# Performance work log

Hardware: AMD Instinct MI355X
Metric: run time of the kernel (lower is better)

Reference implementation:

```python
import jax, jax.numpy as jnp
import numpy as np

B, L, D, V, O = 512, 256, 256, 100000, 1000  # L must equal D (see MaxPool1d(kernel_size=D) + squeeze)


def setup_inputs() -> dict:
    key = jax.random.key(0)
    k1, k2, k3, k4, k5 = jax.random.split(key, 5)
    input_sentence = jax.random.randint(k1, (B, L), 0, V)
    emb_weight = jax.random.normal(k2, (V, D), dtype=jnp.float32) * 0.02
    # xavier_uniform for W_b: bound = sqrt(6/(D+D))
    bound = float(np.sqrt(6.0 / (D + D)))
    W_b = jax.random.uniform(k3, (D, D), dtype=jnp.float32, minval=-bound, maxval=bound)
    lw = float(np.sqrt(1.0 / D))
    lin_w = jax.random.uniform(k4, (O, D), dtype=jnp.float32, minval=-lw, maxval=lw)
    lin_b = jax.random.uniform(k5, (O,), dtype=jnp.float32, minval=-lw, maxval=lw)
    return {"input_sentence": input_sentence, "emb_weight": emb_weight,
            "W_b": W_b, "lin_w": lin_w, "lin_b": lin_b}


def reference(input_sentence, emb_weight, W_b, lin_w, lin_b):
    # Embedding lookup: [B, L, D]
    we = emb_weight[input_sentence]
    # torch stores embeddings as [B, D, L] then re-transposes inside the co-attention;
    # net effect: C = tanh(E W_b E^T) with E = [B, L, D]  ->  C: [B, L, L]
    C = jnp.tanh(jnp.einsum('bld,de,bme->blm', we, W_b, we))
    # Dropout(p=0.5) is identity in eval mode.
    # MaxPool1d(kernel_size=D) over last axis with L == D -> max over last dim, keepdims
    max_cow = jnp.max(C, axis=-1, keepdims=True)          # [B, L, 1]
    a_q = jax.nn.softmax(max_cow, axis=1)                  # softmax over L
    # bmm(a_q^T [B,1,L], E [B,L,D]) -> [B,1,D], then squeeze dim 1
    f_w = jnp.einsum('blo,bld->bod', a_q, we)[:, 0, :]     # [B, D]
    return f_w @ lin_w.T + lin_b                           # [B, O]
```

## Files before the change

kernel.cpp:

```cpp
#include <hip/hip_runtime.h>
#include <hip/hip_bf16.h>
#include <math.h>

#define B_ 512
#define L_ 256
#define D_ 256
#define V_ 100000
#define O_ 1000

typedef __attribute__((ext_vector_type(8))) short short8;
typedef __attribute__((ext_vector_type(4))) float f32x4;

static __device__ __forceinline__ unsigned short f2bf(float f) {
    union { float f; unsigned u; } v; v.f = f;
    unsigned r = v.u + 0x7FFFu + ((v.u >> 16) & 1u);
    return (unsigned short)(r >> 16);
}
static __device__ __forceinline__ float bf2f(unsigned short u) {
    union { unsigned u; float f; } v; v.u = ((unsigned)u) << 16;
    return v.f;
}
static __device__ __forceinline__ short8 pack8(float4 a, float4 c) {
    short8 o;
    o[0] = (short)f2bf(a.x); o[1] = (short)f2bf(a.y);
    o[2] = (short)f2bf(a.z); o[3] = (short)f2bf(a.w);
    o[4] = (short)f2bf(c.x); o[5] = (short)f2bf(c.y);
    o[6] = (short)f2bf(c.z); o[7] = (short)f2bf(c.w);
    return o;
}
static __device__ __forceinline__ int fsw(int d) { return d ^ (((d >> 5) & 7) << 2); }

__global__ __launch_bounds__(256) void k_wt(const float* __restrict__ Wb,
                                            unsigned short* __restrict__ Wbf) {
    int i = blockIdx.x * 256 + threadIdx.x;
    Wbf[i] = f2bf(Wb[i]);
}

__global__ __launch_bounds__(512, 2) void k_attn(const int* __restrict__ tok,
                                                 const float* __restrict__ emb,
                                                 const unsigned short* __restrict__ Wbf,
                                                 float* __restrict__ fw) {
    __shared__ __align__(16) char lds[163840];
    char* EsC = lds;
    char* HtC = lds + 131072;
    float* red2    = (float*)(lds + 131072);
    float* scratch = (float*)(lds + 132096);
    float* fred    = (float*)(lds + 132160);

    int b = blockIdx.x;
    int tid = threadIdx.x;
    int wid = tid >> 6, ln = tid & 63;
    int l16 = ln & 15, gp = ln >> 4;
    int i0 = wid * 32;
    const int* tb = tok + (b << 8);

    short8 wfr[8][2];
#pragma unroll
    for (int k = 0; k < 8; k++)
#pragma unroll
        for (int rf = 0; rf < 2; rf++)
            wfr[k][rf] = *(const short8*)(Wbf + ((i0 + rf * 16 + l16) << 8) + k * 32 + gp * 8);

#pragma unroll
    for (int it = 0; it < 4; it++) {
        int c = it * 512 + tid;
        int row = c >> 5, c16 = c & 31;
        const float4* src = (const float4*)(emb + ((size_t)tb[row] << 8) + (c16 << 3));
        short8 o = pack8(src[0], src[1]);
        *(short8*)(EsC + ((row << 9) | ((c16 << 4) ^ ((row & 7) << 4)))) = o;
    }
    __syncthreads();

    float4 ga[6], gb[6];
#pragma unroll
    for (int it = 0; it < 6; it++) {
        int c = (it + 4) * 512 + tid;
        int row = c >> 5, c16 = c & 31;
        const float4* src = (const float4*)(emb + ((size_t)tb[row] << 8) + (c16 << 3));
        ga[it] = src[0]; gb[it] = src[1];
    }

    float rmax[8];
#pragma unroll
    for (int i = 0; i < 8; i++) rmax[i] = -1e30f;

    auto P1 = [&](int m0) {
        f32x4 acc[2][4] = {};
#pragma unroll
        for (int k0 = 0; k0 < 256; k0 += 32) {
            int kk2 = (k0 + gp * 8) * 2;
            short8 bfr[4];
#pragma unroll
            for (int cf = 0; cf < 4; cf++) {
                int jg = m0 + cf * 16 + l16;
                bfr[cf] = *(const short8*)(EsC + ((jg << 9) | (kk2 ^ ((jg & 7) << 4))));
            }
            int ks = k0 >> 5;
            __builtin_amdgcn_s_setprio(1);
#pragma unroll
            for (int rf = 0; rf < 2; rf++)
#pragma unroll
                for (int cf = 0; cf < 4; cf++)
                    acc[rf][cf] = __builtin_amdgcn_mfma_f32_16x16x32_bf16(
                        wfr[ks][rf], bfr[cf], acc[rf][cf], 0, 0, 0);
            __builtin_amdgcn_s_setprio(0);
        }
#pragma unroll
        for (int rf = 0; rf < 2; rf++)
#pragma unroll
            for (int cf = 0; cf < 4; cf++) {
                int i = i0 + rf * 16 + gp * 4;
                int jl = cf * 16 + l16;
                unsigned long long pk;
                unsigned short* p = (unsigned short*)&pk;
                p[0] = f2bf(acc[rf][cf][0]);
                p[1] = f2bf(acc[rf][cf][1]);
                p[2] = f2bf(acc[rf][cf][2]);
                p[3] = f2bf(acc[rf][cf][3]);
                *(unsigned long long*)(HtC + ((jl << 9) | ((i * 2) ^ ((jl & 7) << 4)))) = pk;
            }
    };

    short8 efr[8][2];
    auto P2 = [&]() {
        f32x4 acc[2][4] = {};
#pragma unroll
        for (int k0 = 0; k0 < 256; k0 += 32) {
            int kk2 = (k0 + gp * 8) * 2;
            short8 bb[4];
#pragma unroll
            for (int cf = 0; cf < 4; cf++) {
                int m = cf * 16 + l16;
                bb[cf] = *(const short8*)(HtC + ((m << 9) | (kk2 ^ ((m & 7) << 4))));
            }
            int ks = k0 >> 5;
            __builtin_amdgcn_s_setprio(1);
#pragma unroll
            for (int rf = 0; rf < 2; rf++)
#pragma unroll
                for (int cf = 0; cf < 4; cf++)
                    acc[rf][cf] = __builtin_amdgcn_mfma_f32_16x16x32_bf16(
                        efr[ks][rf], bb[cf], acc[rf][cf], 0, 0, 0);
            __builtin_amdgcn_s_setprio(0);
        }
#pragma unroll
        for (int rf = 0; rf < 2; rf++)
#pragma unroll
            for (int r = 0; r < 4; r++) {
                float mx = fmaxf(fmaxf(acc[rf][0][r], acc[rf][1][r]),
                                 fmaxf(acc[rf][2][r], acc[rf][3][r]));
                rmax[rf * 4 + r] = fmaxf(rmax[rf * 4 + r], mx);
            }
    };

    P1(0);

#pragma unroll
    for (int it = 0; it < 6; it++) {
        int c = (it + 4) * 512 + tid;
        int row = c >> 5, c16 = c & 31;
        short8 o = pack8(ga[it], gb[it]);
        *(short8*)(EsC + ((row << 9) | ((c16 << 4) ^ ((row & 7) << 4)))) = o;
    }
#pragma unroll
    for (int it = 10; it < 16; it++) {
        int c = it * 512 + tid;
        int row = c >> 5, c16 = c & 31;
        const float4* src = (const float4*)(emb + ((size_t)tb[row] << 8) + (c16 << 3));
        short8 o = pack8(src[0], src[1]);
        *(short8*)(EsC + ((row << 9) | ((c16 << 4) ^ ((row & 7) << 4)))) = o;
    }
    __syncthreads();

#pragma unroll
    for (int k = 0; k < 8; k++)
#pragma unroll
        for (int rf = 0; rf < 2; rf++) {
            int l = i0 + rf * 16 + l16;
            efr[k][rf] = *(const short8*)(EsC + ((l << 9) | ((k * 64 + gp * 16) ^ ((l & 7) << 4))));
        }

    P2();
    __syncthreads();

    for (int mt = 1; mt < 4; mt++) {
        P1(mt * 64);
        __syncthreads();
        P2();
        __syncthreads();
    }

#pragma unroll
    for (int i = 0; i < 8; i++) {
        float v = rmax[i];
        v = fmaxf(v, __shfl_xor(v, 1));
        v = fmaxf(v, __shfl_xor(v, 2));
        v = fmaxf(v, __shfl_xor(v, 4));
        v = fmaxf(v, __shfl_xor(v, 8));
        rmax[i] = v;
    }
    if (l16 == 0) {
#pragma unroll
        for (int rf = 0; rf < 2; rf++)
#pragma unroll
            for (int r = 0; r < 4; r++)
                red2[i0 + rf * 16 + gp * 4 + r] = rmax[rf * 4 + r];
    }
    __syncthreads();

    float x = -1e30f;
    if (tid < 256) x = tanhf(red2[tid]);
    float mx = x;
#pragma unroll
    for (int s = 1; s < 64; s <<= 1) mx = fmaxf(mx, __shfl_xor(mx, s));
    if (ln == 0) scratch[wid] = mx;
    __syncthreads();
    float bm = scratch[0];
#pragma unroll
    for (int i = 1; i < 8; i++) bm = fmaxf(bm, scratch[i]);
    float e = (tid < 256) ? expf(x - bm) : 0.f;
    float sm = e;
#pragma unroll
    for (int s = 1; s < 64; s <<= 1) sm += __shfl_xor(sm, s);
    if (ln == 0) scratch[8 + wid] = sm;
    __syncthreads();
    float tot = 0.f;
#pragma unroll
    for (int i = 0; i < 8; i++) tot += scratch[8 + i];
    if (tid < 256) red2[tid] = e / tot;
    __syncthreads();

    {
        int g = tid >> 5;
        int d0 = (tid & 31) << 3;
        float s0[8] = {0.f, 0.f, 0.f, 0.f, 0.f, 0.f, 0.f, 0.f};
        int lbase = g << 4;
#pragma unroll
        for (int li = 0; li < 16; li++) {
            int l = lbase + li;
            float aql = red2[l];
            int byt = (l << 9) | ((d0 * 2) ^ ((l & 7) << 4));
            short8 v = *(const short8*)(EsC + byt);
#pragma unroll
            for (int jj = 0; jj < 8; jj++)
                s0[jj] += aql * bf2f((unsigned short)v[jj]);
        }
        f32x4 w0, w1;
        w0[0] = s0[0]; w0[1] = s0[1]; w0[2] = s0[2]; w0[3] = s0[3];
        w1[0] = s0[4]; w1[1] = s0[5]; w1[2] = s0[6]; w1[3] = s0[7];
        *(f32x4*)(fred + g * 256 + fsw(d0)) = w0;
        *(f32x4*)(fred + g * 256 + fsw(d0 + 4)) = w1;
    }
    __syncthreads();
    if (tid < 256) {
        float f = 0.f;
        int dw = fsw(tid);
#pragma unroll
        for (int g2 = 0; g2 < 16; g2++) f += fred[g2 * 256 + dw];
        fw[(b << 8) + tid] = f;
    }
}

__global__ __launch_bounds__(256) void k_out(const float* __restrict__ fw,
                                             const float* __restrict__ lw,
                                             const float* __restrict__ lb,
                                             float* __restrict__ out) {
    __shared__ float As[32][68];
    __shared__ float Bs[64][65];
    int tid = threadIdx.x;
    int tx = tid & 15, ty = tid >> 4;
    int r0 = blockIdx.y * 32, n0 = blockIdx.x * 64;
    float acc[2][4] = {};
    for (int k0 = 0; k0 < 256; k0 += 64) {
        __syncthreads();
#pragma unroll
        for (int it = 0; it < 2; it++) {
            int idx = it * 256 + tid;
            int i = idx >> 4, k4 = (idx & 15) << 2;
            *(float4*)&As[i][k4] = *(const float4*)&fw[(r0 + i) * 256 + k0 + k4];
        }
#pragma unroll
        for (int it = 0; it < 4; it++) {
            int idx = it * 256 + tid;
            int n = idx >> 4, k4 = (idx & 15) << 2;
            int nn = n0 + n;
            float4 v = {0.f, 0.f, 0.f, 0.f};
            if (nn < O_) v = *(const float4*)&lw[(size_t)nn * 256 + k0 + k4];
            Bs[k4][n] = v.x; Bs[k4 + 1][n] = v.y; Bs[k4 + 2][n] = v.z; Bs[k4 + 3][n] = v.w;
        }
        __syncthreads();
#pragma unroll
        for (int k = 0; k < 64; k++) {
            float a0 = As[ty * 2][k], a1 = As[ty * 2 + 1][k];
            float b0 = Bs[k][tx * 4], b1 = Bs[k][tx * 4 + 1];
            float b2 = Bs[k][tx * 4 + 2], b3 = Bs[k][tx * 4 + 3];
            acc[0][0] += a0 * b0; acc[0][1] += a0 * b1; acc[0][2] += a0 * b2; acc[0][3] += a0 * b3;
            acc[1][0] += a1 * b0; acc[1][1] += a1 * b1; acc[1][2] += a1 * b2; acc[1][3] += a1 * b3;
        }
    }
#pragma unroll
    for (int i = 0; i < 2; i++)
#pragma unroll
        for (int j = 0; j < 4; j++) {
            int n = n0 + tx * 4 + j;
            if (n < O_) out[(size_t)(r0 + ty * 2 + i) * O_ + n] = acc[i][j] + lb[n];
        }
}

extern "C" void kernel_launch(void* const* d_in, const int* in_sizes, int n_in,
                              void* d_out, int out_size, void* d_ws, size_t ws_size,
                              hipStream_t stream) {
    const int* tok = (const int*)d_in[0];
    const float* emb = (const float*)d_in[1];
    const float* Wb = (const float*)d_in[2];
    const float* lw = (const float*)d_in[3];
    const float* lb = (const float*)d_in[4];
    float* out = (float*)d_out;

    char* ws = (char*)d_ws;
    unsigned short* Wbf = (unsigned short*)(ws);
    float*          fwp = (float*)(ws + 131072);

    hipLaunchKernelGGL(k_wt,   dim3(256),    dim3(256), 0, stream, Wb, Wbf);
    hipLaunchKernelGGL(k_attn, dim3(512),    dim3(512), 0, stream, tok, emb, Wbf, fwp);
    hipLaunchKernelGGL(k_out,  dim3(16, 16), dim3(256), 0, stream, fwp, lw, lb, out);
}
```

Measured before the change: 76.38 us.

## Split attention kernel into producer/consumer warp groups with double-buffered intermediate

```diff
diff --git a/kernel.cpp b/kernel.cpp
--- a/kernel.cpp
+++ b/kernel.cpp
@@ -20,13 +20,16 @@
     union { unsigned u; float f; } v; v.u = ((unsigned)u) << 16;
     return v.f;
 }
-static __device__ __forceinline__ short8 pack8(float4 a, float4 c) {
-    short8 o;
-    o[0] = (short)f2bf(a.x); o[1] = (short)f2bf(a.y);
-    o[2] = (short)f2bf(a.z); o[3] = (short)f2bf(a.w);
-    o[4] = (short)f2bf(c.x); o[5] = (short)f2bf(c.y);
-    o[6] = (short)f2bf(c.z); o[7] = (short)f2bf(c.w);
-    return o;
+static __device__ __forceinline__ unsigned cvtpk(float lo, float hi) {
+    unsigned r;
+    asm("v_cvt_pk_bf16_f32 %0, %1, %2" : "=v"(r) : "v"(lo), "v"(hi));
+    return r;
+}
+static __device__ __forceinline__ short8 pack8c(float4 a, float4 c) {
+    union { unsigned u[4]; short8 s; } o;
+    o.u[0] = cvtpk(a.x, a.y); o.u[1] = cvtpk(a.z, a.w);
+    o.u[2] = cvtpk(c.x, c.y); o.u[3] = cvtpk(c.z, c.w);
+    return o.s;
 }
 static __device__ __forceinline__ int fsw(int d) { return d ^ (((d >> 5) & 7) << 2); }
 
@@ -42,7 +45,6 @@
                                                  float* __restrict__ fw) {
     __shared__ __align__(16) char lds[163840];
     char* EsC = lds;
-    char* HtC = lds + 131072;
     float* red2    = (float*)(lds + 131072);
     float* scratch = (float*)(lds + 132096);
     float* fred    = (float*)(lds + 132160);
@@ -51,160 +53,142 @@
     int tid = threadIdx.x;
     int wid = tid >> 6, ln = tid & 63;
     int l16 = ln & 15, gp = ln >> 4;
-    int i0 = wid * 32;
+    bool prod = (wid < 4);
     const int* tb = tok + (b << 8);
 
-    short8 wfr[8][2];
-#pragma unroll
-    for (int k = 0; k < 8; k++)
-#pragma unroll
-        for (int rf = 0; rf < 2; rf++)
-            wfr[k][rf] = *(const short8*)(Wbf + ((i0 + rf * 16 + l16) << 8) + k * 32 + gp * 8);
+    short8 afr[8][4];
+    if (prod) {
+        int r0 = wid << 6;
+#pragma unroll
+        for (int k = 0; k < 8; k++)
+#pragma unroll
+            for (int rf = 0; rf < 4; rf++)
+                afr[k][rf] = *(const short8*)(Wbf + ((r0 + rf * 16 + l16) << 8) + k * 32 + gp * 8);
+    }
 
 #pragma unroll
     for (int it = 0; it < 4; it++) {
         int c = it * 512 + tid;
         int row = c >> 5, c16 = c & 31;
         const float4* src = (const float4*)(emb + ((size_t)tb[row] << 8) + (c16 << 3));
-        short8 o = pack8(src[0], src[1]);
+        short8 o = pack8c(src[0], src[1]);
         *(short8*)(EsC + ((row << 9) | ((c16 << 4) ^ ((row & 7) << 4)))) = o;
     }
     __syncthreads();
 
-    float4 ga[6], gb[6];
-#pragma unroll
-    for (int it = 0; it < 6; it++) {
-        int c = (it + 4) * 512 + tid;
-        int row = c >> 5, c16 = c & 31;
-        const float4* src = (const float4*)(emb + ((size_t)tb[row] << 8) + (c16 << 3));
-        ga[it] = src[0]; gb[it] = src[1];
-    }
-
-    float rmax[8];
-#pragma unroll
-    for (int i = 0; i < 8; i++) rmax[i] = -1e30f;
-
-    auto P1 = [&](int m0) {
-        f32x4 acc[2][4] = {};
-#pragma unroll
-        for (int k0 = 0; k0 < 256; k0 += 32) {
-            int kk2 = (k0 + gp * 8) * 2;
-            short8 bfr[4];
-#pragma unroll
-            for (int cf = 0; cf < 4; cf++) {
-                int jg = m0 + cf * 16 + l16;
-                bfr[cf] = *(const short8*)(EsC + ((jg << 9) | (kk2 ^ ((jg & 7) << 4))));
+    float rmax[16];
+#pragma unroll
+    for (int i = 0; i < 16; i++) rmax[i] = -1e30f;
+
+    for (int s = 0; s <= 8; s++) {
+        if (prod) {
+            if (s < 8) {
+                char* Ht = lds + 131072 + ((s & 1) << 14);
+                f32x4 acc[4][2] = {};
+#pragma unroll
+                for (int k0 = 0; k0 < 256; k0 += 32) {
+                    int kk2 = (k0 + gp * 8) * 2;
+                    short8 bfr[2];
+#pragma unroll
+                    for (int cf = 0; cf < 2; cf++) {
+                        int jg = s * 32 + cf * 16 + l16;
+                        bfr[cf] = *(const short8*)(EsC + ((jg << 9) | (kk2 ^ ((jg & 7) << 4))));
+                    }
+                    int ks = k0 >> 5;
+                    __builtin_amdgcn_s_setprio(1);
+#pragma unroll
+                    for (int rf = 0; rf < 4; rf++)
+#pragma unroll
+                        for (int cf = 0; cf < 2; cf++)
+                            acc[rf][cf] = __builtin_amdgcn_mfma_f32_16x16x32_bf16(
+                                afr[ks][rf], bfr[cf], acc[rf][cf], 0, 0, 0);
+                    __builtin_amdgcn_s_setprio(0);
+                }
+#pragma unroll
+                for (int rf = 0; rf < 4; rf++)
+#pragma unroll
+                    for (int cf = 0; cf < 2; cf++) {
+                        int i = (wid << 6) + rf * 16 + gp * 4;
+                        int jl = cf * 16 + l16;
+                        unsigned long long pk =
+                            ((unsigned long long)cvtpk(acc[rf][cf][2], acc[rf][cf][3]) << 32)
+                            | cvtpk(acc[rf][cf][0], acc[rf][cf][1]);
+                        *(unsigned long long*)(Ht + ((jl << 9) | ((i * 2) ^ ((jl & 7) << 4)))) = pk;
+                    }
             }
-            int ks = k0 >> 5;
-            __builtin_amdgcn_s_setprio(1);
-#pragma unroll
-            for (int rf = 0; rf < 2; rf++)
-#pragma unroll
-                for (int cf = 0; cf < 4; cf++)
-                    acc[rf][cf] = __builtin_amdgcn_mfma_f32_16x16x32_bf16(
-                        wfr[ks][rf], bfr[cf], acc[rf][cf], 0, 0, 0);
-            __builtin_amdgcn_s_setprio(0);
-        }
-#pragma unroll
-        for (int rf = 0; rf < 2; rf++)
-#pragma unroll
-            for (int cf = 0; cf < 4; cf++) {
-                int i = i0 + rf * 16 + gp * 4;
-                int jl = cf * 16 + l16;
-                unsigned long long pk;
-                unsigned short* p = (unsigned short*)&pk;
-                p[0] = f2bf(acc[rf][cf][0]);
-                p[1] = f2bf(acc[rf][cf][1]);
-                p[2] = f2bf(acc[rf][cf][2]);
-                p[3] = f2bf(acc[rf][cf][3]);
-                *(unsigned long long*)(HtC + ((jl << 9) | ((i * 2) ^ ((jl & 7) << 4)))) = pk;
+        } else {
+            if (s == 0) {
+                int t4 = tid - 256;
+#pragma unroll
+                for (int it = 0; it < 24; it++) {
+                    int c = it * 256 + t4;
+                    int row = 64 + (c >> 5), c16 = c & 31;
+                    const float4* src = (const float4*)(emb + ((size_t)tb[row] << 8) + (c16 << 3));
+                    short8 o = pack8c(src[0], src[1]);
+                    *(short8*)(EsC + ((row << 9) | ((c16 << 4) ^ ((row & 7) << 4)))) = o;
+                }
+            } else {
+                if (s == 1) {
+                    int r0 = (wid - 4) << 6;
+#pragma unroll
+                    for (int k = 0; k < 8; k++)
+#pragma unroll
+                        for (int rf = 0; rf < 4; rf++) {
+                            int l = r0 + rf * 16 + l16;
+                            afr[k][rf] = *(const short8*)(EsC +
+                                ((l << 9) | ((k * 64 + gp * 16) ^ ((l & 7) << 4))));
+                        }
+                }
+                char* Ht = lds + 131072 + (((s - 1) & 1) << 14);
+                f32x4 acc[4][2] = {};
+#pragma unroll
+                for (int k0 = 0; k0 < 256; k0 += 32) {
+                    int kk2 = (k0 + gp * 8) * 2;
+                    short8 bb[2];
+#pragma unroll
+                    for (int cf = 0; cf < 2; cf++) {
+                        int m = cf * 16 + l16;
+                        bb[cf] = *(const short8*)(Ht + ((m << 9) | (kk2 ^ ((m & 7) << 4))));
+                    }
+                    int ks = k0 >> 5;
+                    __builtin_amdgcn_s_setprio(1);
+#pragma unroll
+                    for (int rf = 0; rf < 4; rf++)
+#pragma unroll
+                        for (int cf = 0; cf < 2; cf++)
+                            acc[rf][cf] = __builtin_amdgcn_mfma_f32_16x16x32_bf16(
+                                afr[ks][rf], bb[cf], acc[rf][cf], 0, 0, 0);
+                    __builtin_amdgcn_s_setprio(0);
+                }
+#pragma unroll
+                for (int rf = 0; rf < 4; rf++)
+#pragma unroll
+                    for (int r = 0; r < 4; r++)
+                        rmax[rf * 4 + r] = fmaxf(rmax[rf * 4 + r],
+                                                 fmaxf(acc[rf][0][r], acc[rf][1][r]));
             }
-    };
-
-    short8 efr[8][2];
-    auto P2 = [&]() {
-        f32x4 acc[2][4] = {};
-#pragma unroll
-        for (int k0 = 0; k0 < 256; k0 += 32) {
-            int kk2 = (k0 + gp * 8) * 2;
-            short8 bb[4];
-#pragma unroll
-            for (int cf = 0; cf < 4; cf++) {
-                int m = cf * 16 + l16;
-                bb[cf] = *(const short8*)(HtC + ((m << 9) | (kk2 ^ ((m & 7) << 4))));
-            }
-            int ks = k0 >> 5;
-            __builtin_amdgcn_s_setprio(1);
-#pragma unroll
-            for (int rf = 0; rf < 2; rf++)
-#pragma unroll
-                for (int cf = 0; cf < 4; cf++)
-                    acc[rf][cf] = __builtin_amdgcn_mfma_f32_16x16x32_bf16(
-                        efr[ks][rf], bb[cf], acc[rf][cf], 0, 0, 0);
-            __builtin_amdgcn_s_setprio(0);
-        }
-#pragma unroll
-        for (int rf = 0; rf < 2; rf++)
-#pragma unroll
-            for (int r = 0; r < 4; r++) {
-                float mx = fmaxf(fmaxf(acc[rf][0][r], acc[rf][1][r]),
-                                 fmaxf(acc[rf][2][r], acc[rf][3][r]));
-                rmax[rf * 4 + r] = fmaxf(rmax[rf * 4 + r], mx);
-            }
-    };
-
-    P1(0);
-
-#pragma unroll
-    for (int it = 0; it < 6; it++) {
-        int c = (it + 4) * 512 + tid;
-        int row = c >> 5, c16 = c & 31;
-        short8 o = pack8(ga[it], gb[it]);
-        *(short8*)(EsC + ((row << 9) | ((c16 << 4) ^ ((row & 7) << 4)))) = o;
-    }
-#pragma unroll
-    for (int it = 10; it < 16; it++) {
-        int c = it * 512 + tid;
-        int row = c >> 5, c16 = c & 31;
-        const float4* src = (const float4*)(emb + ((size_t)tb[row] << 8) + (c16 << 3));
-        short8 o = pack8(src[0], src[1]);
-        *(short8*)(EsC + ((row << 9) | ((c16 << 4) ^ ((row & 7) << 4)))) = o;
-    }
-    __syncthreads();
-
-#pragma unroll
-    for (int k = 0; k < 8; k++)
-#pragma unroll
-        for (int rf = 0; rf < 2; rf++) {
-            int l = i0 + rf * 16 + l16;
-            efr[k][rf] = *(const short8*)(EsC + ((l << 9) | ((k * 64 + gp * 16) ^ ((l & 7) << 4))));
-        }
-
-    P2();
-    __syncthreads();
-
-    for (int mt = 1; mt < 4; mt++) {
-        P1(mt * 64);
+        }
         __syncthreads();
-        P2();
-        __syncthreads();
-    }
-
-#pragma unroll
-    for (int i = 0; i < 8; i++) {
-        float v = rmax[i];
-        v = fmaxf(v, __shfl_xor(v, 1));
-        v = fmaxf(v, __shfl_xor(v, 2));
-        v = fmaxf(v, __shfl_xor(v, 4));
-        v = fmaxf(v, __shfl_xor(v, 8));
-        rmax[i] = v;
-    }
-    if (l16 == 0) {
-#pragma unroll
-        for (int rf = 0; rf < 2; rf++)
-#pragma unroll
-            for (int r = 0; r < 4; r++)
-                red2[i0 + rf * 16 + gp * 4 + r] = rmax[rf * 4 + r];
+    }
+
+    if (!prod) {
+#pragma unroll
+        for (int i = 0; i < 16; i++) {
+            float v = rmax[i];
+            v = fmaxf(v, __shfl_xor(v, 1));
+            v = fmaxf(v, __shfl_xor(v, 2));
+            v = fmaxf(v, __shfl_xor(v, 4));
+            v = fmaxf(v, __shfl_xor(v, 8));
+            rmax[i] = v;
+        }
+        if (l16 == 0) {
+            int r0 = (wid - 4) << 6;
+#pragma unroll
+            for (int rf = 0; rf < 4; rf++)
+#pragma unroll
+                for (int r = 0; r < 4; r++)
+                    red2[r0 + rf * 16 + gp * 4 + r] = rmax[rf * 4 + r];
+        }
     }
     __syncthreads();
 
```

New measurement: 299.2 us. +291.7%, slower.

## Software-pipeline the two co-attention GEMM stages over double-buffered 32-column strips

Applied to the files above, without the earlier changes.

```diff
diff --git a/kernel.cpp b/kernel.cpp
--- a/kernel.cpp
+++ b/kernel.cpp
@@ -42,7 +42,6 @@
                                                  float* __restrict__ fw) {
     __shared__ __align__(16) char lds[163840];
     char* EsC = lds;
-    char* HtC = lds + 131072;
     float* red2    = (float*)(lds + 131072);
     float* scratch = (float*)(lds + 132096);
     float* fred    = (float*)(lds + 132160);
@@ -84,31 +83,31 @@
 #pragma unroll
     for (int i = 0; i < 8; i++) rmax[i] = -1e30f;
 
-    auto P1 = [&](int m0) {
-        f32x4 acc[2][4] = {};
+    auto P1strip = [&](int s, char* HtW) {
+        f32x4 acc[2][2] = {};
 #pragma unroll
         for (int k0 = 0; k0 < 256; k0 += 32) {
             int kk2 = (k0 + gp * 8) * 2;
-            short8 bfr[4];
-#pragma unroll
-            for (int cf = 0; cf < 4; cf++) {
-                int jg = m0 + cf * 16 + l16;
-                bfr[cf] = *(const short8*)(EsC + ((jg << 9) | (kk2 ^ ((jg & 7) << 4))));
+            short8 b1[2];
+#pragma unroll
+            for (int cf = 0; cf < 2; cf++) {
+                int jg = s * 32 + cf * 16 + l16;
+                b1[cf] = *(const short8*)(EsC + ((jg << 9) | (kk2 ^ ((jg & 7) << 4))));
             }
             int ks = k0 >> 5;
             __builtin_amdgcn_s_setprio(1);
 #pragma unroll
             for (int rf = 0; rf < 2; rf++)
 #pragma unroll
-                for (int cf = 0; cf < 4; cf++)
+                for (int cf = 0; cf < 2; cf++)
                     acc[rf][cf] = __builtin_amdgcn_mfma_f32_16x16x32_bf16(
-                        wfr[ks][rf], bfr[cf], acc[rf][cf], 0, 0, 0);
+                        wfr[ks][rf], b1[cf], acc[rf][cf], 0, 0, 0);
             __builtin_amdgcn_s_setprio(0);
         }
 #pragma unroll
         for (int rf = 0; rf < 2; rf++)
 #pragma unroll
-            for (int cf = 0; cf < 4; cf++) {
+            for (int cf = 0; cf < 2; cf++) {
                 int i = i0 + rf * 16 + gp * 4;
                 int jl = cf * 16 + l16;
                 unsigned long long pk;
@@ -117,43 +116,41 @@
                 p[1] = f2bf(acc[rf][cf][1]);
                 p[2] = f2bf(acc[rf][cf][2]);
                 p[3] = f2bf(acc[rf][cf][3]);
-                *(unsigned long long*)(HtC + ((jl << 9) | ((i * 2) ^ ((jl & 7) << 4)))) = pk;
+                *(unsigned long long*)(HtW + ((jl << 9) | ((i * 2) ^ ((jl & 7) << 4)))) = pk;
             }
     };
 
     short8 efr[8][2];
-    auto P2 = [&]() {
-        f32x4 acc[2][4] = {};
+    auto P2strip = [&](char* HtR) {
+        f32x4 acc[2][2] = {};
 #pragma unroll
         for (int k0 = 0; k0 < 256; k0 += 32) {
             int kk2 = (k0 + gp * 8) * 2;
-            short8 bb[4];
-#pragma unroll
-            for (int cf = 0; cf < 4; cf++) {
+            short8 b2[2];
+#pragma unroll
+            for (int cf = 0; cf < 2; cf++) {
                 int m = cf * 16 + l16;
-                bb[cf] = *(const short8*)(HtC + ((m << 9) | (kk2 ^ ((m & 7) << 4))));
+                b2[cf] = *(const short8*)(HtR + ((m << 9) | (kk2 ^ ((m & 7) << 4))));
             }
             int ks = k0 >> 5;
             __builtin_amdgcn_s_setprio(1);
 #pragma unroll
             for (int rf = 0; rf < 2; rf++)
 #pragma unroll
-                for (int cf = 0; cf < 4; cf++)
+                for (int cf = 0; cf < 2; cf++)
                     acc[rf][cf] = __builtin_amdgcn_mfma_f32_16x16x32_bf16(
-                        efr[ks][rf], bb[cf], acc[rf][cf], 0, 0, 0);
+                        efr[ks][rf], b2[cf], acc[rf][cf], 0, 0, 0);
             __builtin_amdgcn_s_setprio(0);
         }
 #pragma unroll
         for (int rf = 0; rf < 2; rf++)
 #pragma unroll
-            for (int r = 0; r < 4; r++) {
-                float mx = fmaxf(fmaxf(acc[rf][0][r], acc[rf][1][r]),
-                                 fmaxf(acc[rf][2][r], acc[rf][3][r]));
-                rmax[rf * 4 + r] = fmaxf(rmax[rf * 4 + r], mx);
-            }
+            for (int r = 0; r < 4; r++)
+                rmax[rf * 4 + r] = fmaxf(rmax[rf * 4 + r],
+                                         fmaxf(acc[rf][0][r], acc[rf][1][r]));
     };
 
-    P1(0);
+    P1strip(0, lds + 131072);
 
 #pragma unroll
     for (int it = 0; it < 6; it++) {
@@ -180,15 +177,59 @@
             efr[k][rf] = *(const short8*)(EsC + ((l << 9) | ((k * 64 + gp * 16) ^ ((l & 7) << 4))));
         }
 
-    P2();
-    __syncthreads();
-
-    for (int mt = 1; mt < 4; mt++) {
-        P1(mt * 64);
+    for (int s = 1; s < 8; s++) {
+        char* HtW = lds + 131072 + ((s & 1) << 14);
+        char* HtR = lds + 131072 + (((s - 1) & 1) << 14);
+        f32x4 a1[2][2] = {};
+        f32x4 a2[2][2] = {};
+#pragma unroll
+        for (int k0 = 0; k0 < 256; k0 += 32) {
+            int kk2 = (k0 + gp * 8) * 2;
+            short8 b1[2], b2[2];
+#pragma unroll
+            for (int cf = 0; cf < 2; cf++) {
+                int jg = s * 32 + cf * 16 + l16;
+                b1[cf] = *(const short8*)(EsC + ((jg << 9) | (kk2 ^ ((jg & 7) << 4))));
+                int m = cf * 16 + l16;
+                b2[cf] = *(const short8*)(HtR + ((m << 9) | (kk2 ^ ((m & 7) << 4))));
+            }
+            int ks = k0 >> 5;
+            __builtin_amdgcn_s_setprio(1);
+#pragma unroll
+            for (int rf = 0; rf < 2; rf++)
+#pragma unroll
+                for (int cf = 0; cf < 2; cf++) {
+                    a1[rf][cf] = __builtin_amdgcn_mfma_f32_16x16x32_bf16(
+                        wfr[ks][rf], b1[cf], a1[rf][cf], 0, 0, 0);
+                    a2[rf][cf] = __builtin_amdgcn_mfma_f32_16x16x32_bf16(
+                        efr[ks][rf], b2[cf], a2[rf][cf], 0, 0, 0);
+                }
+            __builtin_amdgcn_s_setprio(0);
+        }
+#pragma unroll
+        for (int rf = 0; rf < 2; rf++)
+#pragma unroll
+            for (int cf = 0; cf < 2; cf++) {
+                int i = i0 + rf * 16 + gp * 4;
+                int jl = cf * 16 + l16;
+                unsigned long long pk;
+                unsigned short* p = (unsigned short*)&pk;
+                p[0] = f2bf(a1[rf][cf][0]);
+                p[1] = f2bf(a1[rf][cf][1]);
+                p[2] = f2bf(a1[rf][cf][2]);
+                p[3] = f2bf(a1[rf][cf][3]);
+                *(unsigned long long*)(HtW + ((jl << 9) | ((i * 2) ^ ((jl & 7) << 4)))) = pk;
+            }
+#pragma unroll
+        for (int rf = 0; rf < 2; rf++)
+#pragma unroll
+            for (int r = 0; r < 4; r++)
+                rmax[rf * 4 + r] = fmaxf(rmax[rf * 4 + r],
+                                         fmaxf(a2[rf][0][r], a2[rf][1][r]));
         __syncthreads();
-        P2();
-        __syncthreads();
-    }
+    }
+
+    P2strip(lds + 131072 + (1 << 14));
 
 #pragma unroll
     for (int i = 0; i < 8; i++) {
@@ -199,6 +240,7 @@
         v = fmaxf(v, __shfl_xor(v, 8));
         rmax[i] = v;
     }
+    __syncthreads();
     if (l16 == 0) {
 #pragma unroll
         for (int rf = 0; rf < 2; rf++)
```

Result: slower. 79.17 us (+3.7%).
